# Kernel tuning notes

Measured on AMD Instinct MI355X. Metric: run time of the kernel, lower is better.

## Reference

```python
import jax, jax.numpy as jnp
import numpy as np

D = 1024      # embed_dim
H = 1365      # expert_hidden_dim = int(4096 / (select_top_k + num_shared_experts)) = int(4096/3)
E = 7         # num_experts = base_num_experts*factor - num_shared = 8 - 1
K = 2         # select_top_k
S_EXP = 1     # num_shared_experts
ALPHA = 0.01
C_Z = 0.001


def setup_inputs() -> dict:
    key = jax.random.key(0)
    ks = jax.random.split(key, 8)
    scaled = lambda k, shape, fan: jax.random.normal(k, shape, jnp.float32) * (1.0 / np.sqrt(fan))
    return {
        "x": jax.random.normal(ks[0], (4, 512, D), jnp.float32),
        "Wg": scaled(ks[1], (E, D), D),            # router weight (no bias)
        "W1": scaled(ks[2], (E, H, D), D),          # routed experts ffn[0] weight
        "b1": jnp.zeros((E, H), jnp.float32),
        "W2": scaled(ks[3], (E, D, H), H),          # routed experts ffn[3] weight
        "b2": jnp.zeros((E, D), jnp.float32),
        "Ws1": scaled(ks[4], (S_EXP, H, D), D),     # shared experts
        "bs1": jnp.zeros((S_EXP, H), jnp.float32),
        "Ws2": scaled(ks[5], (S_EXP, D, H), H),
        "bs2": jnp.zeros((S_EXP, D), jnp.float32),
    }


def _moe_forward(x, Wg, W1, b1, W2, b2, Ws1, bs1, Ws2, bs2):
    B, S, _ = x.shape
    xf = x.reshape(-1, D)                               # [N, D] flattened tokens
    N = xf.shape[0]

    # Gate (eval mode: no router noise, no dropout)
    logits = jnp.einsum('nd,ed->ne', xf, Wg)            # [N, E]
    dense_gate = jax.nn.softmax(logits, axis=-1)
    topk_logits, topk_idx = jax.lax.top_k(logits, K)    # [N, K]
    topk_w = jax.nn.softmax(topk_logits, axis=-1)       # [N, K]

    # Dense gate matrix: weight for selected experts, 0 elsewhere (equivalent to
    # the sorted dispatch + per-expert FFN + index_add combine in the original).
    gates = jnp.zeros((N, E), xf.dtype).at[jnp.arange(N)[:, None], topk_idx].set(topk_w)

    # Routed experts: exact GELU (approximate='none')
    h = jax.nn.gelu(jnp.einsum('nd,ehd->enh', xf, W1) + b1[:, None, :], approximate=False)  # [E, N, H]
    y = jnp.einsum('enh,edh->end', h, W2) + b2[:, None, :]                                  # [E, N, D]
    routed = jnp.einsum('ne,end->nd', gates, y)                                             # [N, D]

    # Shared experts (applied to every token, summed)
    hs = jax.nn.gelu(jnp.einsum('nd,shd->snh', xf, Ws1) + bs1[:, None, :], approximate=False)
    shared = jnp.einsum('snh,sdh->nd', hs, Ws2) + bs2.sum(0)

    final = (routed + shared).reshape(B, S, D)

    # Aux losses
    counts = jnp.zeros((E,), jnp.float32).at[topk_idx.reshape(-1)].add(1.0)  # bincount (non-diff, like torch long)
    dispatch_fraction = jax.lax.stop_gradient(counts) / (N * K)
    l_aux = ALPHA * E * jnp.sum(dispatch_fraction * dense_gate.mean(axis=0))
    cz_lz = C_Z * jnp.mean(jax.nn.logsumexp(logits, axis=-1) ** 2)
    return final, l_aux, cz_lz


def reference(x, Wg, W1, b1, W2, b2, Ws1, bs1, Ws2, bs2):
    return _moe_forward(x, Wg, W1, b1, W2, b2, Ws1, bs1, Ws2, bs2)
```

## Files before the change

kernel.cpp:

```cpp
#include <hip/hip_runtime.h>
#include <hip/hip_bf16.h>
#include <math.h>

typedef unsigned short u16;
typedef __attribute__((ext_vector_type(8))) short bf16x8;
typedef __attribute__((ext_vector_type(4))) float f32x4;

constexpr int D_ = 1024;
constexpr int H_ = 1365;
constexpr int E_ = 7;
constexpr int NTOK = 2048;
constexpr int HP = 1408;
constexpr int NE = 8;
constexpr int SHARED_BASE = 4096;
constexpr int SLOTS = 6144;

#define CI_COUNT 0
#define CI_OFF   8

constexpr size_t WS_CTRL = 0;
constexpr size_t WS_TIDX = 256;
constexpr size_t WS_TW   = WS_TIDX + (size_t)NTOK*2*4;
constexpr size_t WS_PROB = WS_TW   + (size_t)NTOK*2*4;
constexpr size_t WS_LSE2 = WS_PROB + (size_t)NTOK*8*4;
constexpr size_t WS_STOK = WS_LSE2 + (size_t)NTOK*4;
constexpr size_t WS_SW   = WS_STOK + (size_t)SLOTS*4;
constexpr size_t WS_B1   = WS_SW   + (size_t)SLOTS*4;
constexpr size_t WS_B2   = WS_B1   + (size_t)NE*H_*4;
constexpr size_t WS_XB   = ((WS_B2 + (size_t)NE*D_*4) + 255) & ~(size_t)255;
constexpr size_t WS_W1B  = WS_XB  + (size_t)NTOK*D_*2;
constexpr size_t WS_W2B  = WS_W1B + (size_t)NE*H_*D_*2;
constexpr size_t WS_HEB  = WS_W2B + (size_t)NE*D_*HP*2;

__device__ __forceinline__ u16 f2bf(float f) {
    __hip_bfloat16 h = __float2bfloat16(f);
    return __builtin_bit_cast(u16, h);
}

__device__ __forceinline__ void gload_lds16(const u16* g, u16* l) {
    __builtin_amdgcn_global_load_lds(
        (const __attribute__((address_space(1))) void*)g,
        (__attribute__((address_space(3))) void*)l, 16, 0, 0);
}

__device__ __forceinline__ uint4 pack8(float4 a, float4 b) {
    union { u16 h[8]; uint4 v; } u;
    u.h[0]=f2bf(a.x); u.h[1]=f2bf(a.y); u.h[2]=f2bf(a.z); u.h[3]=f2bf(a.w);
    u.h[4]=f2bf(b.x); u.h[5]=f2bf(b.y); u.h[6]=f2bf(b.z); u.h[7]=f2bf(b.w);
    return u.v;
}

__device__ __forceinline__ float fast_gelu(float v) {
    float u = 0.7978845608f * v * (1.f + 0.044715f * v * v);
    float e = __expf(2.f * u);
    float t = 1.f - 2.f / (e + 1.f);
    return 0.5f * v * (1.f + t);
}

#define BM 128
#define BN 128
#define KSTEP 64
#define ATILE (BM*KSTEP)

#define MFMA16(a,b,c) __builtin_amdgcn_mfma_f32_16x16x32_bf16(a, b, c, 0, 0, 0)

template<bool USE_STOK>
__device__ __forceinline__ void gemm1_body(u16* As, u16* Bs,
    const u16* xb, const u16* w1e, const float* b1e,
    const int* stok, int offset, int m0, int valid, int nt,
    u16* heb)
{
    int t = threadIdx.x, wid = t >> 6, lane = t & 63;
    int rl = lane >> 3, cl = lane & 7;
    int sg = cl ^ rl;

    const u16* aP[2]; const u16* bP[2]; int dOff[2];
    #pragma unroll
    for (int c = 0; c < 2; c++) {
        int row = wid*16 + c*8 + rl;
        int ar = min(row, valid-1);
        int tok = USE_STOK ? stok[offset + m0 + ar] : (m0 + ar);
        aP[c] = xb + (size_t)tok*D_ + sg*8;
        int jg = min(nt*BN + row, H_-1);
        bP[c] = w1e + (size_t)jg*D_ + sg*8;
        dOff[c] = (wid*16 + c*8)*KSTEP;
    }

    int wm = (wid >> 2)*64, wn = (wid & 3)*32;
    int frow = lane & 15, kgrp = lane >> 4, swz = frow & 7;
    f32x4 acc[4][2] = {};

    constexpr int nIter = D_/KSTEP;
    for (int tt = 0; tt < nIter; ++tt) {
        __syncthreads();
        int ko = tt*KSTEP;
        #pragma unroll
        for (int c = 0; c < 2; c++) {
            gload_lds16(aP[c]+ko, As + dOff[c]);
            gload_lds16(bP[c]+ko, Bs + dOff[c]);
        }
        __syncthreads();
        __builtin_amdgcn_s_setprio(1);
        #pragma unroll
        for (int s = 0; s < 2; s++) {
            int cc = ((s*4 + kgrp) ^ swz) * 8;
            bf16x8 af[4], bf[2];
            #pragma unroll
            for (int mf = 0; mf < 4; mf++)
                af[mf] = *(const bf16x8*)&As[(wm + mf*16 + frow)*KSTEP + cc];
            #pragma unroll
            for (int nf = 0; nf < 2; nf++)
                bf[nf] = *(const bf16x8*)&Bs[(wn + nf*16 + frow)*KSTEP + cc];
            #pragma unroll
            for (int mf = 0; mf < 4; mf++)
                #pragma unroll
                for (int nf = 0; nf < 2; nf++)
                    acc[mf][nf] = MFMA16(af[mf], bf[nf], acc[mf][nf]);
        }
        __builtin_amdgcn_s_setprio(0);
    }

    int r4 = (lane >> 4)*4, cEl = lane & 15;
    #pragma unroll
    for (int nf = 0; nf < 2; nf++) {
        int gcol = nt*BN + wn + nf*16 + cEl;
        bool cok = gcol < H_;
        float bias = cok ? b1e[gcol] : 0.f;
        #pragma unroll
        for (int mf = 0; mf < 4; mf++) {
            #pragma unroll
            for (int r = 0; r < 4; r++) {
                int row = wm + mf*16 + r4 + r;
                if (row < valid) {
                    float v = 0.f;
                    if (cok) v = fast_gelu(acc[mf][nf][r] + bias);
                    heb[(size_t)(offset + m0 + row)*HP + gcol] = f2bf(v);
                }
            }
        }
    }
}

template<int MODE>
__device__ __forceinline__ void gemm2_body(u16* As, u16* Bs,
    const u16* heb, const u16* w2e, const float* b2e, const float* sw,
    int offset, int m0, int valid, int nt, float* out, const int* stok)
{
    int t = threadIdx.x, wid = t >> 6, lane = t & 63;
    int rl = lane >> 3, cl = lane & 7;
    int sg = cl ^ rl;

    const u16* aP[2]; const u16* bP[2]; int dOff[2];
    #pragma unroll
    for (int c = 0; c < 2; c++) {
        int row = wid*16 + c*8 + rl;
        int ar = min(row, valid-1);
        aP[c] = heb + (size_t)(offset + m0 + ar)*HP + sg*8;
        int jg = nt*BN + row;
        bP[c] = w2e + (size_t)jg*HP + sg*8;
        dOff[c] = (wid*16 + c*8)*KSTEP;
    }

    int wm = (wid >> 2)*64, wn = (wid & 3)*32;
    int frow = lane & 15, kgrp = lane >> 4, swz = frow & 7;
    f32x4 acc[4][2] = {};

    constexpr int nIter = HP/KSTEP;
    for (int tt = 0; tt < nIter; ++tt) {
        __syncthreads();
        int ko = tt*KSTEP;
        #pragma unroll
        for (int c = 0; c < 2; c++) {
            gload_lds16(aP[c]+ko, As + dOff[c]);
            gload_lds16(bP[c]+ko, Bs + dOff[c]);
        }
        __syncthreads();
        __builtin_amdgcn_s_setprio(1);
        #pragma unroll
        for (int s = 0; s < 2; s++) {
            int cc = ((s*4 + kgrp) ^ swz) * 8;
            bf16x8 af[4], bf[2];
            #pragma unroll
            for (int mf = 0; mf < 4; mf++)
                af[mf] = *(const bf16x8*)&As[(wm + mf*16 + frow)*KSTEP + cc];
            #pragma unroll
            for (int nf = 0; nf < 2; nf++)
                bf[nf] = *(const bf16x8*)&Bs[(wn + nf*16 + frow)*KSTEP + cc];
            #pragma unroll
            for (int mf = 0; mf < 4; mf++)
                #pragma unroll
                for (int nf = 0; nf < 2; nf++)
                    acc[mf][nf] = MFMA16(af[mf], bf[nf], acc[mf][nf]);
        }
        __builtin_amdgcn_s_setprio(0);
    }

    int r4 = (lane >> 4)*4, cEl = lane & 15;
    #pragma unroll
    for (int nf = 0; nf < 2; nf++) {
        int gcol = nt*BN + wn + nf*16 + cEl;
        float bias = b2e[gcol];
        #pragma unroll
        for (int mf = 0; mf < 4; mf++) {
            #pragma unroll
            for (int r = 0; r < 4; r++) {
                int row = wm + mf*16 + r4 + r;
                if (row < valid) {
                    if (MODE == 0) {
                        out[(size_t)(m0 + row)*D_ + gcol] = acc[mf][nf][r] + bias;
                    } else {
                        int slot = offset + m0 + row;
                        atomicAdd(out + (size_t)stok[slot]*D_ + gcol,
                                  sw[slot]*(acc[mf][nf][r] + bias));
                    }
                }
            }
        }
    }
}

__device__ void finalize_body(char* big, char* small,
    const int* tidx, const float* tw, const float* probs, const float* lse2,
    int* ci, int* stok, float* sw, float* out)
{
    int*   lt   = (int*)big;
    float* psum = (float*)small;
    float* lsum = (float*)(small + 32);
    int*   cntS = (int*)(small + 64);
    int*   offS = (int*)(small + 96);
    int t = threadIdx.x;
    if (t < 8) { psum[t] = 0.f; cntS[t] = 0; }
    if (t == 0) *lsum = 0.f;
    for (int i = t; i < NTOK*2; i += 512) lt[i] = tidx[i];
    __syncthreads();
    float lp[E_] = {}; float ll = 0.f;
    for (int n = t; n < NTOK; n += 512) {
        #pragma unroll
        for (int e = 0; e < E_; e++) lp[e] += probs[n*8+e];
        ll += lse2[n];
    }
    #pragma unroll
    for (int e = 0; e < E_; e++) atomicAdd(&psum[e], lp[e]);
    atomicAdd(lsum, ll);
    int wid = t >> 6, lane = t & 63;
    if (wid < 7) {
        int c = 0;
        for (int i = lane; i < NTOK*2; i += 64) c += (lt[i] == wid) ? 1 : 0;
        #pragma unroll
        for (int m = 32; m >= 1; m >>= 1) c += __shfl_xor(c, m);
        if (lane == 0) cntS[wid] = c;
    } else {
        for (int n = lane; n < NTOK; n += 64) {
            stok[SHARED_BASE+n] = n; sw[SHARED_BASE+n] = 1.f;
        }
    }
    __syncthreads();
    if (t == 0) {
        int o = 0;
        for (int e = 0; e < E_; e++) { offS[e] = o; o += cntS[e]; }
        offS[7] = SHARED_BASE; cntS[7] = NTOK;
        float la = 0.f;
        for (int e = 0; e < E_; e++)
            la += ((float)cntS[e] / (float)(NTOK*2)) * (psum[e] / (float)NTOK);
        out[(size_t)NTOK*D_]     = 0.01f * 7.f * la;
        out[(size_t)NTOK*D_ + 1] = 0.001f * (*lsum) / (float)NTOK;
        #pragma unroll
        for (int e = 0; e < 8; e++) { ci[CI_COUNT+e] = cntS[e]; ci[CI_OFF+e] = offS[e]; }
    }
    __syncthreads();
    if (wid < 7) {
        int base = offS[wid], run = 0;
        for (int c0 = 0; c0 < NTOK*2; c0 += 64) {
            bool m = (lt[c0 + lane] == wid);
            unsigned long long bal = __ballot(m);
            int pre = __popcll(bal & ((1ull << lane) - 1ull));
            if (m) {
                int i = c0 + lane;
                int s = base + run + pre;
                stok[s] = i >> 1; sw[s] = tw[i];
            }
            run += __popcll(bal);
        }
    }
}

__global__ void prep_kernel(
    const float* __restrict__ x, const float* __restrict__ Wg,
    const float* __restrict__ W1, const float* __restrict__ Ws1,
    const float* __restrict__ b1, const float* __restrict__ bs1,
    int* __restrict__ tidx, float* __restrict__ tw,
    float* __restrict__ probs, float* __restrict__ lse2,
    u16* __restrict__ xb, u16* __restrict__ w1b, float* __restrict__ b1all)
{
    int b = blockIdx.x;
    if (b < 512) {
        int wid = threadIdx.x >> 6, lane = threadIdx.x & 63;
        int n = b*4 + wid;
        float p[E_] = {};
        const float* xr = x + (size_t)n*D_;
        u16* xbr = xb + (size_t)n*D_;
        #pragma unroll
        for (int j = 0; j < 4; j++) {
            int d0 = lane*4 + j*256;
            float4 xv = *(const float4*)(xr + d0);
            ushort4 h;
            h.x = f2bf(xv.x); h.y = f2bf(xv.y); h.z = f2bf(xv.z); h.w = f2bf(xv.w);
            *(ushort4*)(xbr + d0) = h;
            #pragma unroll
            for (int e = 0; e < E_; e++) {
                float4 wv = *(const float4*)(Wg + e*D_ + d0);
                p[e] += xv.x*wv.x + xv.y*wv.y + xv.z*wv.z + xv.w*wv.w;
            }
        }
        #pragma unroll
        for (int e = 0; e < E_; e++) {
            float v = p[e];
            #pragma unroll
            for (int m = 32; m >= 1; m >>= 1) v += __shfl_xor(v, m);
            p[e] = v;
        }
        if (lane == 0) {
            float mx = p[0];
            #pragma unroll
            for (int e = 1; e < E_; e++) mx = fmaxf(mx, p[e]);
            float pr[E_], sum = 0.f;
            #pragma unroll
            for (int e = 0; e < E_; e++) { pr[e] = __expf(p[e]-mx); sum += pr[e]; }
            float lse = mx + logf(sum);
            int i0 = 0;
            #pragma unroll
            for (int e = 1; e < E_; e++) if (p[e] > p[i0]) i0 = e;
            int i1 = -1;
            #pragma unroll
            for (int e = 0; e < E_; e++) if (e != i0 && (i1 < 0 || p[e] > p[i1])) i1 = e;
            float g = expf(p[i1] - p[i0]);
            tidx[n*2] = i0; tidx[n*2+1] = i1;
            tw[n*2] = 1.f/(1.f+g); tw[n*2+1] = g/(1.f+g);
            float inv = 1.f/sum;
            #pragma unroll
            for (int e = 0; e < E_; e++) probs[n*8+e] = pr[e]*inv;
            lse2[n] = lse*lse;
        }
        return;
    }
    const unsigned G1 = (unsigned)(NE*H_*D_/8);
    const unsigned NT = 1536u*256u;
    const unsigned W1FLAT = 7u*(unsigned)(H_*D_);
    unsigned tid = (unsigned)(b-512)*256u + threadIdx.x;
    unsigned i0 = tid, i1 = tid + NT, i2 = tid + 2u*NT, i3 = tid + 3u*NT;
    bool p3 = i3 < G1;
    float4 va0, vb0, va1, vb1, va2, vb2, va3, vb3;
    {
        const float* s0 = (i0*8u < W1FLAT) ? W1 + (size_t)i0*8u : Ws1 + ((size_t)i0*8u - W1FLAT);
        va0 = *(const float4*)s0; vb0 = *(const float4*)(s0+4);
        const float* s1 = (i1*8u < W1FLAT) ? W1 + (size_t)i1*8u : Ws1 + ((size_t)i1*8u - W1FLAT);
        va1 = *(const float4*)s1; vb1 = *(const float4*)(s1+4);
        const float* s2 = (i2*8u < W1FLAT) ? W1 + (size_t)i2*8u : Ws1 + ((size_t)i2*8u - W1FLAT);
        va2 = *(const float4*)s2; vb2 = *(const float4*)(s2+4);
        if (p3) {
            const float* s3 = (i3*8u < W1FLAT) ? W1 + (size_t)i3*8u : Ws1 + ((size_t)i3*8u - W1FLAT);
            va3 = *(const float4*)s3; vb3 = *(const float4*)(s3+4);
        }
    }
    ((uint4*)w1b)[i0] = pack8(va0, vb0);
    ((uint4*)w1b)[i1] = pack8(va1, vb1);
    ((uint4*)w1b)[i2] = pack8(va2, vb2);
    if (p3) ((uint4*)w1b)[i3] = pack8(va3, vb3);
    if (tid < 10920u) b1all[tid] = (tid < 9555u) ? b1[tid] : bs1[tid - 9555u];
}

__global__ __launch_bounds__(512, 8) void k2_kernel(
    const float* __restrict__ W2, const float* __restrict__ Ws2,
    const float* __restrict__ b2, const float* __restrict__ bs2,
    u16* __restrict__ w2b, float* __restrict__ b2all,
    const int* __restrict__ tidx, const float* __restrict__ tw,
    const float* __restrict__ probs, const float* __restrict__ lse2,
    int* __restrict__ ci, int* __restrict__ stok, float* __restrict__ sw,
    float* __restrict__ out,
    const u16* __restrict__ xb, const u16* __restrict__ w1b,
    const float* __restrict__ b1all, u16* __restrict__ heb)
{
    __shared__ u16 As[ATILE];
    __shared__ u16 Bs[ATILE];
    int b = blockIdx.x;
    if (b == 0) {
        finalize_body((char*)As, (char*)Bs, tidx, tw, probs, lse2, ci, stok, sw, out);
        return;
    }
    if (b <= 176) {
        int tdx = b - 1;
        int mt = tdx/11, nt = tdx - mt*11;
        gemm1_body<false>(As, Bs, xb, w1b + (size_t)7*H_*D_, b1all + 7*H_,
                          nullptr, SHARED_BASE, mt*BM, BM, nt, heb);
        return;
    }
    unsigned tid = (unsigned)(b-177)*512u + threadIdx.x;
    if (tid < 8192u) b2all[tid] = (tid < 7168u) ? b2[tid] : bs2[tid - 7168u];
    int lane = threadIdx.x & 63;
    int rw0 = (((b-177)*8) + (threadIdx.x >> 6)) * 2;
    #pragma unroll
    for (int j = 0; j < 2; j++) {
        int rw = rw0 + j;
        int ec = rw >> 10, drow = rw & 1023;
        const float* src = (ec < 7) ? (W2 + ((size_t)ec*D_ + drow)*(size_t)H_)
                                    : (Ws2 + (size_t)drow*(size_t)H_);
        u16* dst = w2b + (size_t)rw*HP;
        #pragma unroll
        for (int h0 = 0; h0 < HP; h0 += 64) {
            int h = h0 + lane;
            float v = (h < H_) ? src[h] : 0.f;
            dst[h] = f2bf(v);
        }
    }
}

__global__ __launch_bounds__(512, 8) void k3_kernel(
    const int* __restrict__ ci, const int* __restrict__ stok,
    const u16* __restrict__ xb, const u16* __restrict__ w1b,
    const float* __restrict__ b1all, u16* __restrict__ heb,
    const u16* __restrict__ w2b, const float* __restrict__ b2all,
    float* __restrict__ out)
{
    __shared__ u16 As[ATILE];
    __shared__ u16 Bs[ATILE];
    int x = blockIdx.x, yb = blockIdx.y;
    if (yb < 176) {
        if (x == 7) return;
        int e = x, mt = yb/11, nt = yb - mt*11;
        int count = ci[CI_COUNT+e];
        int m0 = mt*BM;
        if (m0 >= count) return;
        gemm1_body<true>(As, Bs, xb, w1b + (size_t)e*H_*D_, b1all + e*H_,
                         stok, ci[CI_OFF+e], m0, min(BM, count-m0), nt, heb);
    } else {
        int idx = (yb - 176)*8 + x;
        int mt = idx >> 3, nt = idx & 7;
        gemm2_body<0>(As, Bs, heb, w2b + (size_t)7*D_*HP, b2all + 7*D_,
                      nullptr, SHARED_BASE, mt*BM, BM, nt, out, nullptr);
    }
}

__global__ __launch_bounds__(512, 8) void k4_kernel(
    const int* __restrict__ ci, const int* __restrict__ stok, const float* __restrict__ sw,
    const u16* __restrict__ heb, const u16* __restrict__ w2b,
    const float* __restrict__ b2all, float* __restrict__ out)
{
    __shared__ u16 As[ATILE];
    __shared__ u16 Bs[ATILE];
    int x = blockIdx.x;
    if (x == 7) return;
    int yb = blockIdx.y;
    int e = x, mt = yb >> 3, nt = yb & 7;
    int count = ci[CI_COUNT+e];
    int m0 = mt*BM;
    if (m0 >= count) return;
    gemm2_body<1>(As, Bs, heb, w2b + (size_t)e*D_*HP, b2all + e*D_,
                  sw, ci[CI_OFF+e], m0, min(BM, count-m0), nt, out, stok);
}

extern "C" void kernel_launch(void* const* d_in, const int* in_sizes, int n_in,
                              void* d_out, int out_size, void* d_ws, size_t ws_size,
                              hipStream_t stream)
{
    const float* x   = (const float*)d_in[0];
    const float* Wg  = (const float*)d_in[1];
    const float* W1  = (const float*)d_in[2];
    const float* b1  = (const float*)d_in[3];
    const float* W2  = (const float*)d_in[4];
    const float* b2  = (const float*)d_in[5];
    const float* Ws1 = (const float*)d_in[6];
    const float* bs1 = (const float*)d_in[7];
    const float* Ws2 = (const float*)d_in[8];
    const float* bs2 = (const float*)d_in[9];
    float* out = (float*)d_out;
    char* ws = (char*)d_ws;

    int*   ci    = (int*)(ws + WS_CTRL);
    int*   tidx  = (int*)(ws + WS_TIDX);
    float* tw    = (float*)(ws + WS_TW);
    float* probs = (float*)(ws + WS_PROB);
    float* lse2  = (float*)(ws + WS_LSE2);
    int*   stok  = (int*)(ws + WS_STOK);
    float* sw    = (float*)(ws + WS_SW);
    float* b1all = (float*)(ws + WS_B1);
    float* b2all = (float*)(ws + WS_B2);
    u16*   xb    = (u16*)(ws + WS_XB);
    u16*   w1b   = (u16*)(ws + WS_W1B);
    u16*   w2b   = (u16*)(ws + WS_W2B);
    u16*   heb   = (u16*)(ws + WS_HEB);

    prep_kernel<<<2048, 256, 0, stream>>>(x, Wg, W1, Ws1, b1, bs1,
                                          tidx, tw, probs, lse2, xb, w1b, b1all);
    k2_kernel<<<689, 512, 0, stream>>>(W2, Ws2, b2, bs2, w2b, b2all,
                                       tidx, tw, probs, lse2, ci, stok, sw, out,
                                       xb, w1b, b1all, heb);
    k3_kernel<<<dim3(8, 176 + 16), 512, 0, stream>>>(ci, stok, xb, w1b, b1all, heb,
                                                     w2b, b2all, out);
    k4_kernel<<<dim3(8, 128), 512, 0, stream>>>(ci, stok, sw, heb, w2b, b2all, out);
}
```

Baseline: 137.4 us.

## Reschedule shared-expert GEMMs into the routed GEMM kernels and combine via atomics

Moves the shared-expert first GEMM out of the weight-conversion kernel and into the routed first-GEMM kernel. Moves the shared-expert second GEMM into the routed second-GEMM kernel, where it accumulates through atomicAdd, and zeroes the output with a memset up front. The aim is to keep the conversion kernel lightweight and balance GEMM work across the later launches, so idle tails shrink. In exchange it adds a memset and turns the shared-expert output writes into atomics, which depends on the shared-slot token and weight entries being set correctly.

```diff
diff --git a/kernel.cpp b/kernel.cpp
--- a/kernel.cpp
+++ b/kernel.cpp
@@ -141,7 +141,6 @@
     }
 }
 
-template<int MODE>
 __device__ __forceinline__ void gemm2_body(u16* As, u16* Bs,
     const u16* heb, const u16* w2e, const float* b2e, const float* sw,
     int offset, int m0, int valid, int nt, float* out, const int* stok)
@@ -206,13 +205,9 @@
             for (int r = 0; r < 4; r++) {
                 int row = wm + mf*16 + r4 + r;
                 if (row < valid) {
-                    if (MODE == 0) {
-                        out[(size_t)(m0 + row)*D_ + gcol] = acc[mf][nf][r] + bias;
-                    } else {
-                        int slot = offset + m0 + row;
-                        atomicAdd(out + (size_t)stok[slot]*D_ + gcol,
-                                  sw[slot]*(acc[mf][nf][r] + bias));
-                    }
+                    int slot = offset + m0 + row;
+                    atomicAdd(out + (size_t)stok[slot]*D_ + gcol,
+                              sw[slot]*(acc[mf][nf][r] + bias));
                 }
             }
         }
@@ -376,28 +371,19 @@
     const int* __restrict__ tidx, const float* __restrict__ tw,
     const float* __restrict__ probs, const float* __restrict__ lse2,
     int* __restrict__ ci, int* __restrict__ stok, float* __restrict__ sw,
-    float* __restrict__ out,
-    const u16* __restrict__ xb, const u16* __restrict__ w1b,
-    const float* __restrict__ b1all, u16* __restrict__ heb)
-{
-    __shared__ u16 As[ATILE];
-    __shared__ u16 Bs[ATILE];
+    float* __restrict__ out)
+{
+    __shared__ char smA[16384];
+    __shared__ char smB[128];
     int b = blockIdx.x;
     if (b == 0) {
-        finalize_body((char*)As, (char*)Bs, tidx, tw, probs, lse2, ci, stok, sw, out);
+        finalize_body(smA, smB, tidx, tw, probs, lse2, ci, stok, sw, out);
         return;
     }
-    if (b <= 176) {
-        int tdx = b - 1;
-        int mt = tdx/11, nt = tdx - mt*11;
-        gemm1_body<false>(As, Bs, xb, w1b + (size_t)7*H_*D_, b1all + 7*H_,
-                          nullptr, SHARED_BASE, mt*BM, BM, nt, heb);
-        return;
-    }
-    unsigned tid = (unsigned)(b-177)*512u + threadIdx.x;
+    unsigned tid = (unsigned)(b-1)*512u + threadIdx.x;
     if (tid < 8192u) b2all[tid] = (tid < 7168u) ? b2[tid] : bs2[tid - 7168u];
     int lane = threadIdx.x & 63;
-    int rw0 = (((b-177)*8) + (threadIdx.x >> 6)) * 2;
+    int rw0 = (((b-1)*8) + (threadIdx.x >> 6)) * 2;
     #pragma unroll
     for (int j = 0; j < 2; j++) {
         int rw = rw0 + j;
@@ -417,9 +403,7 @@
 __global__ __launch_bounds__(512, 8) void k3_kernel(
     const int* __restrict__ ci, const int* __restrict__ stok,
     const u16* __restrict__ xb, const u16* __restrict__ w1b,
-    const float* __restrict__ b1all, u16* __restrict__ heb,
-    const u16* __restrict__ w2b, const float* __restrict__ b2all,
-    float* __restrict__ out)
+    const float* __restrict__ b1all, u16* __restrict__ heb)
 {
     __shared__ u16 As[ATILE];
     __shared__ u16 Bs[ATILE];
@@ -434,9 +418,9 @@
                          stok, ci[CI_OFF+e], m0, min(BM, count-m0), nt, heb);
     } else {
         int idx = (yb - 176)*8 + x;
-        int mt = idx >> 3, nt = idx & 7;
-        gemm2_body<0>(As, Bs, heb, w2b + (size_t)7*D_*HP, b2all + 7*D_,
-                      nullptr, SHARED_BASE, mt*BM, BM, nt, out, nullptr);
+        int mt = idx/11, nt = idx - mt*11;
+        gemm1_body<false>(As, Bs, xb, w1b + (size_t)7*H_*D_, b1all + 7*H_,
+                          nullptr, SHARED_BASE, mt*BM, BM, nt, heb);
     }
 }
 
@@ -447,15 +431,21 @@
 {
     __shared__ u16 As[ATILE];
     __shared__ u16 Bs[ATILE];
-    int x = blockIdx.x;
-    if (x == 7) return;
-    int yb = blockIdx.y;
-    int e = x, mt = yb >> 3, nt = yb & 7;
-    int count = ci[CI_COUNT+e];
-    int m0 = mt*BM;
-    if (m0 >= count) return;
-    gemm2_body<1>(As, Bs, heb, w2b + (size_t)e*D_*HP, b2all + e*D_,
-                  sw, ci[CI_OFF+e], m0, min(BM, count-m0), nt, out, stok);
+    int x = blockIdx.x, yb = blockIdx.y;
+    if (yb < 128) {
+        if (x == 7) return;
+        int e = x, mt = yb >> 3, nt = yb & 7;
+        int count = ci[CI_COUNT+e];
+        int m0 = mt*BM;
+        if (m0 >= count) return;
+        gemm2_body(As, Bs, heb, w2b + (size_t)e*D_*HP, b2all + e*D_,
+                   sw, ci[CI_OFF+e], m0, min(BM, count-m0), nt, out, stok);
+    } else {
+        int idx = (yb - 128)*8 + x;
+        int mt = idx >> 3, nt = idx & 7;
+        gemm2_body(As, Bs, heb, w2b + (size_t)7*D_*HP, b2all + 7*D_,
+                   sw, SHARED_BASE, mt*BM, BM, nt, out, stok);
+    }
 }
 
 extern "C" void kernel_launch(void* const* d_in, const int* in_sizes, int n_in,
@@ -489,12 +479,12 @@
     u16*   w2b   = (u16*)(ws + WS_W2B);
     u16*   heb   = (u16*)(ws + WS_HEB);
 
+    hipMemsetAsync(d_out, 0, (size_t)out_size*sizeof(float), stream);
+
     prep_kernel<<<2048, 256, 0, stream>>>(x, Wg, W1, Ws1, b1, bs1,
                                           tidx, tw, probs, lse2, xb, w1b, b1all);
-    k2_kernel<<<689, 512, 0, stream>>>(W2, Ws2, b2, bs2, w2b, b2all,
-                                       tidx, tw, probs, lse2, ci, stok, sw, out,
-                                       xb, w1b, b1all, heb);
-    k3_kernel<<<dim3(8, 176 + 16), 512, 0, stream>>>(ci, stok, xb, w1b, b1all, heb,
-                                                     w2b, b2all, out);
-    k4_kernel<<<dim3(8, 128), 512, 0, stream>>>(ci, stok, sw, heb, w2b, b2all, out);
-}
+    k2_kernel<<<513, 512, 0, stream>>>(W2, Ws2, b2, bs2, w2b, b2all,
+                                       tidx, tw, probs, lse2, ci, stok, sw, out);
+    k3_kernel<<<dim3(8, 176 + 22), 512, 0, stream>>>(ci, stok, xb, w1b, b1all, heb);
+    k4_kernel<<<dim3(8, 128 + 16), 512, 0, stream>>>(ci, stok, sw, heb, w2b, b2all, out);
+}
```

New measurement: 164.2 us. 19.5% more time.

## Move routed W2 bf16 conversion from k2 into k3 to overlap with GEMMs

Applied to the files above, without the earlier changes.

Only the shared-expert W2 rows are converted in k2 now, and the 7 routed experts' W2 fp32→bf16 conversion moves into extra blocks of k3. Those blocks run alongside the routed GEMM1 and shared GEMM2 work. The aim is to shorten k2 and hide the memory-bound weight conversion behind compute in k3, since routed W2 is only needed by k4. The risk is that the conversion blocks compete with the GEMM blocks for bandwidth and CU slots in k3.

```diff
diff --git a/kernel.cpp b/kernel.cpp
--- a/kernel.cpp
+++ b/kernel.cpp
@@ -370,8 +370,8 @@
 }
 
 __global__ __launch_bounds__(512, 8) void k2_kernel(
-    const float* __restrict__ W2, const float* __restrict__ Ws2,
-    const float* __restrict__ b2, const float* __restrict__ bs2,
+    const float* __restrict__ Ws2, const float* __restrict__ b2,
+    const float* __restrict__ bs2,
     u16* __restrict__ w2b, float* __restrict__ b2all,
     const int* __restrict__ tidx, const float* __restrict__ tw,
     const float* __restrict__ probs, const float* __restrict__ lse2,
@@ -397,14 +397,12 @@
     unsigned tid = (unsigned)(b-177)*512u + threadIdx.x;
     if (tid < 8192u) b2all[tid] = (tid < 7168u) ? b2[tid] : bs2[tid - 7168u];
     int lane = threadIdx.x & 63;
-    int rw0 = (((b-177)*8) + (threadIdx.x >> 6)) * 2;
+    int rs0 = (((b-177)*8) + (threadIdx.x >> 6)) * 2;
     #pragma unroll
     for (int j = 0; j < 2; j++) {
-        int rw = rw0 + j;
-        int ec = rw >> 10, drow = rw & 1023;
-        const float* src = (ec < 7) ? (W2 + ((size_t)ec*D_ + drow)*(size_t)H_)
-                                    : (Ws2 + (size_t)drow*(size_t)H_);
-        u16* dst = w2b + (size_t)rw*HP;
+        int rs = rs0 + j;
+        const float* src = Ws2 + (size_t)rs*(size_t)H_;
+        u16* dst = w2b + (size_t)(7*D_ + rs)*HP;
         #pragma unroll
         for (int h0 = 0; h0 < HP; h0 += 64) {
             int h = h0 + lane;
@@ -418,7 +416,8 @@
     const int* __restrict__ ci, const int* __restrict__ stok,
     const u16* __restrict__ xb, const u16* __restrict__ w1b,
     const float* __restrict__ b1all, u16* __restrict__ heb,
-    const u16* __restrict__ w2b, const float* __restrict__ b2all,
+    const float* __restrict__ W2, u16* __restrict__ w2b,
+    const u16* __restrict__ w2b_c, const float* __restrict__ b2all,
     float* __restrict__ out)
 {
     __shared__ u16 As[ATILE];
@@ -432,11 +431,28 @@
         if (m0 >= count) return;
         gemm1_body<true>(As, Bs, xb, w1b + (size_t)e*H_*D_, b1all + e*H_,
                          stok, ci[CI_OFF+e], m0, min(BM, count-m0), nt, heb);
-    } else {
+    } else if (yb < 192) {
         int idx = (yb - 176)*8 + x;
         int mt = idx >> 3, nt = idx & 7;
-        gemm2_body<0>(As, Bs, heb, w2b + (size_t)7*D_*HP, b2all + 7*D_,
+        gemm2_body<0>(As, Bs, heb, w2b_c + (size_t)7*D_*HP, b2all + 7*D_,
                       nullptr, SHARED_BASE, mt*BM, BM, nt, out, nullptr);
+    } else {
+        int idx = (yb - 192)*8 + x;
+        int lane = threadIdx.x & 63;
+        int rw0 = idx*16 + (threadIdx.x >> 6)*2;
+        #pragma unroll
+        for (int j = 0; j < 2; j++) {
+            int rw = rw0 + j;
+            int ec = rw >> 10, drow = rw & 1023;
+            const float* src = W2 + ((size_t)ec*D_ + drow)*(size_t)H_;
+            u16* dst = w2b + (size_t)rw*HP;
+            #pragma unroll
+            for (int h0 = 0; h0 < HP; h0 += 64) {
+                int h = h0 + lane;
+                float v = (h < H_) ? src[h] : 0.f;
+                dst[h] = f2bf(v);
+            }
+        }
     }
 }
 
@@ -491,10 +507,10 @@
 
     prep_kernel<<<2048, 256, 0, stream>>>(x, Wg, W1, Ws1, b1, bs1,
                                           tidx, tw, probs, lse2, xb, w1b, b1all);
-    k2_kernel<<<689, 512, 0, stream>>>(W2, Ws2, b2, bs2, w2b, b2all,
+    k2_kernel<<<241, 512, 0, stream>>>(Ws2, b2, bs2, w2b, b2all,
                                        tidx, tw, probs, lse2, ci, stok, sw, out,
                                        xb, w1b, b1all, heb);
-    k3_kernel<<<dim3(8, 176 + 16), 512, 0, stream>>>(ci, stok, xb, w1b, b1all, heb,
-                                                     w2b, b2all, out);
+    k3_kernel<<<dim3(8, 176 + 16 + 56), 512, 0, stream>>>(ci, stok, xb, w1b, b1all, heb,
+                                                          W2, w2b, w2b, b2all, out);
     k4_kernel<<<dim3(8, 128), 512, 0, stream>>>(ci, stok, sw, heb, w2b, b2all, out);
 }
```

Measured after the change: 137.0 us. About the same (-0.3%).
